# Optimization experiments

Hardware: AMD Instinct MI355X
Metric: run time of the kernel (lower is better)

## Reference

```python
import jax, jax.numpy as jnp
import numpy as np

N = 65536      # nodes
E = 262144     # edges per metapath
K = 8          # sampled edges per node
NMP = 2        # metapaths (n_mp)
DEPTH = 2      # layers
H = 4          # heads
D = 256        # prep_len / hidden (= H*PH)
PH = 64        # per-head output dim
ED = 64        # raw edge embedding dim


def setup_inputs() -> dict:
    key = jax.random.key(0)
    ks = jax.random.split(key, 16)
    s = 1.0 / np.sqrt(D)
    return {
        "feats": jax.random.normal(ks[0], (N, D), jnp.float32),
        "edge_emb": jax.random.normal(ks[1], (NMP, E, ED), jnp.float32),
        "edge_node_adj": jax.random.randint(ks[2], (NMP, E, 2), 0, N, dtype=jnp.int32),
        "node2edge_idx": jax.random.randint(ks[3], (NMP, N, K), 0, E, dtype=jnp.int32),
        "W_prep0": jax.random.normal(ks[4], (D, D), jnp.float32) * s,
        "W_prep1": jax.random.normal(ks[5], (D, D), jnp.float32) * s,
        "W_eprep": jax.random.normal(ks[6], (NMP, ED, D), jnp.float32) * (1.0 / np.sqrt(ED)),
        "a_e": jax.random.normal(ks[7], (NMP, DEPTH, H, D), jnp.float32) * s,
        "a_n": jax.random.normal(ks[8], (NMP, DEPTH, H, D), jnp.float32) * s,
        "W_e": jax.random.normal(ks[9], (NMP, DEPTH, H, D, PH), jnp.float32) * s,
        "a_s": jax.random.normal(ks[10], (NMP, DEPTH, H, D), jnp.float32) * s,
        "a_edge": jax.random.normal(ks[11], (NMP, DEPTH, H, D), jnp.float32) * s,
        "W_self": jax.random.normal(ks[12], (NMP, DEPTH, H, D, PH), jnp.float32) * s,
        "W_nb": jax.random.normal(ks[13], (NMP, DEPTH, H, D, PH), jnp.float32) * s,
    }


def _forward(feats, edge_emb, edge_node_adj, node2edge_idx,
             W_prep0, W_prep1, W_eprep, a_e, a_n, W_e, a_s, a_edge, W_self, W_nb):
    dummy = feats @ W_prep0     # prep(layer_idx=0)  [N,D]
    base = feats @ W_prep1      # prep(layer_idx=1)  [N,D]
    outputs = []
    for mp in range(NMP):
        x = base
        edges = edge_emb[mp] @ W_eprep[mp]           # [E,D]
        ena = edge_node_adj[mp]                      # [E,2]
        n2e = node2edge_idx[mp]                      # [N,K]
        skips = []
        for L in range(DEPTH):
            # --- edge aggregator: gather 2 endpoint node feats, attend, project ---
            ep = x[ena]                              # [E,2,D] gather
            s_e = jax.nn.leaky_relu(
                jnp.einsum('eqd,hd->ehq', ep, a_n[mp, L])
                + jnp.einsum('ed,hd->eh', edges, a_e[mp, L])[..., None], 0.2)  # [E,H,2]
            alp = jax.nn.softmax(s_e, axis=-1)
            agg = jnp.einsum('ehq,eqd->ehd', alp, ep)                          # [E,H,D]
            e_out = jax.nn.elu(
                jnp.einsum('ehd,hdp->ehp', edges[:, None, :] + agg, W_e[mp, L])
            ).reshape(E, H * PH)                                               # [E,D]
            # --- node aggregator: gather K sampled edge feats (OLD edges), attend ---
            xin = x if L > 0 else dummy              # layer 0 self-feature uses dummy prep
            eg = edges[n2e]                          # [N,K,D] gather
            s_n = jax.nn.leaky_relu(
                jnp.einsum('nd,hd->nh', xin, a_s[mp, L])[:, :, None]
                + jnp.einsum('nkd,hd->nhk', eg, a_edge[mp, L]), 0.2)           # [N,H,K]
            aln = jax.nn.softmax(s_n, axis=-1)
            nag = jnp.einsum('nhk,nkd->nhd', aln, eg)                          # [N,H,D]
            n_out = jax.nn.elu(
                jnp.einsum('nd,hdp->nhp', xin, W_self[mp, L])
                + jnp.einsum('nhd,hdp->nhp', nag, W_nb[mp, L])
            ).reshape(N, H * PH)                                               # [N,D]
            skips.append(n_out)
            x = n_out
            edges = e_out
        outputs.append(jnp.concatenate(skips, axis=-1))   # [N, DEPTH*D]
    return jnp.stack(outputs, axis=0)                     # [NMP, N, DEPTH*D]


def reference(feats, edge_emb, edge_node_adj, node2edge_idx,
              W_prep0, W_prep1, W_eprep, a_e, a_n, W_e, a_s, a_edge, W_self, W_nb):
    return _forward(feats, edge_emb, edge_node_adj, node2edge_idx,
                    W_prep0, W_prep1, W_eprep, a_e, a_n, W_e, a_s, a_edge, W_self, W_nb)
```

## Files before the change

kernel.cpp:

```cpp
#include <hip/hip_runtime.h>

typedef unsigned short ushort_t;
typedef unsigned int uint_t;

#define N_NODES 65536
#define N_EDGES 262144

typedef __attribute__((ext_vector_type(8))) short bf16x8;
typedef __attribute__((ext_vector_type(4))) float f32x4;

__device__ __forceinline__ ushort_t f2b(float x) {
  uint_t u = __float_as_uint(x);
  u += 0x7fffu + ((u >> 16) & 1u);
  return (ushort_t)(u >> 16);
}
__device__ __forceinline__ void dec8(uint4 v, float* f) {
  f[0] = __uint_as_float(v.x << 16); f[1] = __uint_as_float(v.x & 0xffff0000u);
  f[2] = __uint_as_float(v.y << 16); f[3] = __uint_as_float(v.y & 0xffff0000u);
  f[4] = __uint_as_float(v.z << 16); f[5] = __uint_as_float(v.z & 0xffff0000u);
  f[6] = __uint_as_float(v.w << 16); f[7] = __uint_as_float(v.w & 0xffff0000u);
}
__device__ __forceinline__ void dec4(uint2 v, float* f) {
  f[0] = __uint_as_float(v.x << 16); f[1] = __uint_as_float(v.x & 0xffff0000u);
  f[2] = __uint_as_float(v.y << 16); f[3] = __uint_as_float(v.y & 0xffff0000u);
}
__device__ __forceinline__ uint4 enc8(const float* f) {
  uint4 v;
  v.x = (uint_t)f2b(f[0]) | ((uint_t)f2b(f[1]) << 16);
  v.y = (uint_t)f2b(f[2]) | ((uint_t)f2b(f[3]) << 16);
  v.z = (uint_t)f2b(f[4]) | ((uint_t)f2b(f[5]) << 16);
  v.w = (uint_t)f2b(f[6]) | ((uint_t)f2b(f[7]) << 16);
  return v;
}
__device__ __forceinline__ uint2 enc4(const float* f) {
  uint2 v;
  v.x = (uint_t)f2b(f[0]) | ((uint_t)f2b(f[1]) << 16);
  v.y = (uint_t)f2b(f[2]) | ((uint_t)f2b(f[3]) << 16);
  return v;
}
__device__ __forceinline__ void ld8(const float* p, float* f) {
  float4 v0 = *(const float4*)p;
  float4 v1 = *(const float4*)(p + 4);
  f[0]=v0.x; f[1]=v0.y; f[2]=v0.z; f[3]=v0.w;
  f[4]=v1.x; f[5]=v1.y; f[6]=v1.z; f[7]=v1.w;
}

#define ELUF(v) ((v) > 0.f ? (v) : __expf(v) - 1.f)

__device__ __forceinline__ void async16(void* lds, const void* g) {
  __builtin_amdgcn_global_load_lds(
      (const __attribute__((address_space(1))) void*)g,
      (__attribute__((address_space(3))) void*)lds, 16, 0, 0);
}

__global__ void wt_kernel(const float* __restrict__ src, ushort_t* __restrict__ dst,
                          int K, int N) {
  long m = blockIdx.y;
  long base = m * (long)K * N;
  int tid = blockIdx.x * 256 + threadIdx.x;
  if (tid >= K * N) return;
  int k = tid % K, n = tid / K;
  dst[base + (long)n * K + k] = f2b(src[base + (long)k * N + n]);
}

__global__ __launch_bounds__(256, 2) void gemm_mfma2(
    const float* __restrict__ A, const ushort_t* __restrict__ Wt0,
    const ushort_t* __restrict__ Wt1, ushort_t* __restrict__ out0,
    ushort_t* __restrict__ out1) {
  __shared__ __align__(16) char smem[4096 + 16384 + 16384];
  ushort_t (*sA)[32]  = (ushort_t(*)[32])smem;
  ushort_t (*sB0)[32] = (ushort_t(*)[32])(smem + 4096);
  ushort_t (*sB1)[32] = (ushort_t(*)[32])(smem + 20480);
  int t = threadIdx.x, w = t >> 6, l = t & 63;
  long r0 = (long)blockIdx.x * 64;
  f32x4 zero = {0.f, 0.f, 0.f, 0.f};
  f32x4 acc0[4][4], acc1[4][4];
#pragma unroll
  for (int mt = 0; mt < 4; ++mt)
#pragma unroll
    for (int nt = 0; nt < 4; ++nt) { acc0[mt][nt] = zero; acc1[mt][nt] = zero; }

  for (int kc = 0; kc < 8; ++kc) {
    __syncthreads();
    {
      int r = t >> 2, ks8 = (t & 3) * 8;
      float f[8]; ld8(A + (r0 + r) * 256 + kc * 32 + ks8, f);
      *(uint4*)&sA[r][ks8] = enc8(f);
    }
#pragma unroll
    for (int j = 0; j < 4; ++j) {
      int u = (w * 4 + j) * 64 + l;
      int n = u >> 2, ks = u & 3;
      async16((char*)sB0 + (w * 4 + j) * 1024, Wt0 + (long)n * 256 + kc * 32 + ks * 8);
      async16((char*)sB1 + (w * 4 + j) * 1024, Wt1 + (long)n * 256 + kc * 32 + ks * 8);
    }
    __syncthreads();
    bf16x8 af[4];
#pragma unroll
    for (int mt = 0; mt < 4; ++mt)
      af[mt] = *(const bf16x8*)&sA[mt * 16 + (l & 15)][(l >> 4) * 8];
#pragma unroll
    for (int nt = 0; nt < 4; ++nt) {
      bf16x8 b0 = *(const bf16x8*)&sB0[w * 64 + nt * 16 + (l & 15)][(l >> 4) * 8];
      bf16x8 b1 = *(const bf16x8*)&sB1[w * 64 + nt * 16 + (l & 15)][(l >> 4) * 8];
#pragma unroll
      for (int mt = 0; mt < 4; ++mt) {
        acc0[mt][nt] = __builtin_amdgcn_mfma_f32_16x16x32_bf16(af[mt], b0, acc0[mt][nt], 0, 0, 0);
        acc1[mt][nt] = __builtin_amdgcn_mfma_f32_16x16x32_bf16(af[mt], b1, acc1[mt][nt], 0, 0, 0);
      }
    }
  }
#pragma unroll
  for (int mt = 0; mt < 4; ++mt)
#pragma unroll
    for (int nt = 0; nt < 4; ++nt)
#pragma unroll
      for (int i = 0; i < 4; ++i) {
        long row = r0 + mt * 16 + (l >> 4) * 4 + i;
        int col = w * 64 + nt * 16 + (l & 15);
        out0[row * 256 + col] = f2b(acc0[mt][nt][i]);
        out1[row * 256 + col] = f2b(acc1[mt][nt][i]);
      }
}

__global__ __launch_bounds__(256, 2) void gemm_eproj(
    const ushort_t* __restrict__ A, const ushort_t* __restrict__ Wt,
    const float* __restrict__ a_vec,
    ushort_t* __restrict__ outb, float* __restrict__ sco) {
  __shared__ __align__(16) char smem[4096 + 16384 + 8192];
  ushort_t (*sA)[32]   = (ushort_t(*)[32])smem;
  ushort_t (*sB)[32]   = (ushort_t(*)[32])(smem + 4096);
  ushort_t (*sAe)[256] = (ushort_t(*)[256])(smem + 20480);
  int t = threadIdx.x, w = t >> 6, l = t & 63;
  long r0 = (long)blockIdx.x * 64;

  {
    int row = t >> 4, seg = (t & 15) * 16;
    float f[16];
    if (row < 4) {
      ld8(a_vec + row * 256 + seg, f);
      ld8(a_vec + row * 256 + seg + 8, f + 8);
    } else {
#pragma unroll
      for (int i = 0; i < 16; ++i) f[i] = 0.f;
    }
    *(uint4*)&sAe[row][seg] = enc8(f);
    *(uint4*)&sAe[row][seg + 8] = enc8(f + 8);
  }

  f32x4 zero = {0.f, 0.f, 0.f, 0.f};
  f32x4 acc[4][4];
  f32x4 accs[4];
#pragma unroll
  for (int mt = 0; mt < 4; ++mt) {
    accs[mt] = zero;
#pragma unroll
    for (int nt = 0; nt < 4; ++nt) acc[mt][nt] = zero;
  }

  for (int kc = 0; kc < 8; ++kc) {
    __syncthreads();
    async16((char*)sA + w * 1024, A + (r0 + (t >> 2)) * 256 + kc * 32 + (t & 3) * 8);
#pragma unroll
    for (int j = 0; j < 4; ++j) {
      int u = (w * 4 + j) * 64 + l;
      int n = u >> 2, ks = u & 3;
      async16((char*)sB + (w * 4 + j) * 1024, Wt + (long)n * 256 + kc * 32 + ks * 8);
    }
    __syncthreads();
    bf16x8 af[4], bf[4];
#pragma unroll
    for (int mt = 0; mt < 4; ++mt)
      af[mt] = *(const bf16x8*)&sA[mt * 16 + (l & 15)][(l >> 4) * 8];
#pragma unroll
    for (int nt = 0; nt < 4; ++nt)
      bf[nt] = *(const bf16x8*)&sB[w * 64 + nt * 16 + (l & 15)][(l >> 4) * 8];
#pragma unroll
    for (int mt = 0; mt < 4; ++mt)
#pragma unroll
      for (int nt = 0; nt < 4; ++nt)
        acc[mt][nt] = __builtin_amdgcn_mfma_f32_16x16x32_bf16(af[mt], bf[nt], acc[mt][nt], 0, 0, 0);
    if (w == 0) {
      bf16x8 bs = *(const bf16x8*)&sAe[l & 15][kc * 32 + (l >> 4) * 8];
#pragma unroll
      for (int mt = 0; mt < 4; ++mt)
        accs[mt] = __builtin_amdgcn_mfma_f32_16x16x32_bf16(af[mt], bs, accs[mt], 0, 0, 0);
    }
  }
#pragma unroll
  for (int mt = 0; mt < 4; ++mt)
#pragma unroll
    for (int nt = 0; nt < 4; ++nt)
#pragma unroll
      for (int i = 0; i < 4; ++i) {
        long row = r0 + mt * 16 + (l >> 4) * 4 + i;
        int col = w * 64 + nt * 16 + (l & 15);
        outb[row * 256 + col] = f2b(acc[mt][nt][i]);
      }
  if (w == 0 && (l & 15) < 4) {
#pragma unroll
    for (int mt = 0; mt < 4; ++mt)
#pragma unroll
      for (int i = 0; i < 4; ++i) {
        long row = r0 + mt * 16 + (l >> 4) * 4 + i;
        sco[row * 4 + (l & 15)] = accs[mt][i];
      }
  }
}

__global__ __launch_bounds__(256, 2) void edge_mega(
    const float* __restrict__ eemb,
    const ushort_t* __restrict__ WtEp,
    const ushort_t* __restrict__ WtN0,
    const ushort_t* __restrict__ WtE0,
    const ushort_t* __restrict__ WtN1,
    const float* __restrict__ a_e0,
    const float* __restrict__ a_ed0,
    const float* __restrict__ a_ed1,
    const int* __restrict__ ena,
    const ushort_t* __restrict__ xprojE,
    const float* __restrict__ xan,
    ushort_t* __restrict__ eproj0, float* __restrict__ sed0,
    ushort_t* __restrict__ eprojL1, float* __restrict__ sed1) {
  __shared__ __align__(16) char smem[32768 + 16384 + 8192 + 4096 + 1024 + 2048 + 512];
  char* sEc            = smem;
  ushort_t (*sB)[32]   = (ushort_t(*)[32])(smem + 32768);
  ushort_t (*sAe)[256] = (ushort_t(*)[256])(smem + 49152);
  ushort_t (*sT)[32]   = (ushort_t(*)[32])(smem + 57344);
  float* sSea          = (float*)(smem + 61440);
  float (*sAlp)[4][2]  = (float(*)[4][2])(smem + 62464);
  int* sIdx            = (int*)(smem + 64512);
  int t = threadIdx.x, w = t >> 6, l = t & 63;
  long e0 = (long)blockIdx.x * 64;

  if (t < 128) sIdx[t] = ena[e0 * 2 + t];
  {
    int row = t >> 4, seg = (t & 15) * 16;
    float f[16];
    if (row < 8) {
      const float* src = (row < 4 ? a_e0 + row * 256 : a_ed0 + (row - 4) * 256) + seg;
      ld8(src, f); ld8(src + 8, f + 8);
    } else {
#pragma unroll
      for (int i = 0; i < 16; ++i) f[i] = 0.f;
    }
    *(uint4*)&sAe[row][seg] = enc8(f);
    *(uint4*)&sAe[row][seg + 8] = enc8(f + 8);
  }

  f32x4 zero = {0.f, 0.f, 0.f, 0.f};
  f32x4 acc[4][4];
#pragma unroll
  for (int mt = 0; mt < 4; ++mt)
#pragma unroll
    for (int nt = 0; nt < 4; ++nt) acc[mt][nt] = zero;

  for (int kc = 0; kc < 2; ++kc) {
    __syncthreads();
    {
      int r = t >> 2, ks8 = (t & 3) * 8;
      float f[8]; ld8(eemb + (e0 + r) * 64 + kc * 32 + ks8, f);
      *(uint4*)&sT[r][ks8] = enc8(f);
    }
#pragma unroll
    for (int j = 0; j < 4; ++j) {
      int u = (w * 4 + j) * 64 + l;
      int n = u >> 2, ks = u & 3;
      async16((char*)sB + (w * 4 + j) * 1024, WtEp + (long)n * 64 + kc * 32 + ks * 8);
    }
    __syncthreads();
    bf16x8 af[4], bf[4];
#pragma unroll
    for (int mt = 0; mt < 4; ++mt)
      af[mt] = *(const bf16x8*)&sT[mt * 16 + (l & 15)][(l >> 4) * 8];
#pragma unroll
    for (int nt = 0; nt < 4; ++nt)
      bf[nt] = *(const bf16x8*)&sB[w * 64 + nt * 16 + (l & 15)][(l >> 4) * 8];
#pragma unroll
    for (int mt = 0; mt < 4; ++mt)
#pragma unroll
      for (int nt = 0; nt < 4; ++nt)
        acc[mt][nt] = __builtin_amdgcn_mfma_f32_16x16x32_bf16(af[mt], bf[nt], acc[mt][nt], 0, 0, 0);
  }
#pragma unroll
  for (int mt = 0; mt < 4; ++mt)
#pragma unroll
    for (int nt = 0; nt < 4; ++nt)
#pragma unroll
      for (int i = 0; i < 4; ++i) {
        int row = mt * 16 + (l >> 4) * 4 + i;
        int col = w * 64 + nt * 16 + (l & 15);
        int cb = (col >> 3) ^ ((row & 7) << 2);
        *(ushort_t*)(sEc + row * 512 + cb * 16 + (col & 7) * 2) = f2b(acc[mt][nt][i]);
      }

  f32x4 accs[4];
#pragma unroll
  for (int mt = 0; mt < 4; ++mt) {
    accs[mt] = zero;
#pragma unroll
    for (int nt = 0; nt < 4; ++nt) acc[mt][nt] = zero;
  }
  for (int kc = 0; kc < 8; ++kc) {
    __syncthreads();
#pragma unroll
    for (int j = 0; j < 4; ++j) {
      int u = (w * 4 + j) * 64 + l;
      int n = u >> 2, ks = u & 3;
      async16((char*)sB + (w * 4 + j) * 1024, WtN0 + (long)n * 256 + kc * 32 + ks * 8);
    }
    __syncthreads();
    bf16x8 af[4], bf[4];
#pragma unroll
    for (int mt = 0; mt < 4; ++mt) {
      int row = mt * 16 + (l & 15);
      int cb = (kc * 4 + (l >> 4)) ^ ((row & 7) << 2);
      af[mt] = *(const bf16x8*)(sEc + row * 512 + cb * 16);
    }
#pragma unroll
    for (int nt = 0; nt < 4; ++nt)
      bf[nt] = *(const bf16x8*)&sB[w * 64 + nt * 16 + (l & 15)][(l >> 4) * 8];
#pragma unroll
    for (int mt = 0; mt < 4; ++mt)
#pragma unroll
      for (int nt = 0; nt < 4; ++nt)
        acc[mt][nt] = __builtin_amdgcn_mfma_f32_16x16x32_bf16(af[mt], bf[nt], acc[mt][nt], 0, 0, 0);
    if (w == 0) {
      bf16x8 bs = *(const bf16x8*)&sAe[l & 15][kc * 32 + (l >> 4) * 8];
#pragma unroll
      for (int mt = 0; mt < 4; ++mt)
        accs[mt] = __builtin_amdgcn_mfma_f32_16x16x32_bf16(af[mt], bs, accs[mt], 0, 0, 0);
    }
  }
  __syncthreads();
#pragma unroll
  for (int mt = 0; mt < 4; ++mt)
#pragma unroll
    for (int nt = 0; nt < 4; ++nt)
#pragma unroll
      for (int i = 0; i < 4; ++i) {
        long row = e0 + mt * 16 + (l >> 4) * 4 + i;
        int col = w * 64 + nt * 16 + (l & 15);
        eproj0[row * 256 + col] = f2b(acc[mt][nt][i]);
      }
  if (w == 0) {
    int c = l & 15;
#pragma unroll
    for (int mt = 0; mt < 4; ++mt)
#pragma unroll
      for (int i = 0; i < 4; ++i) {
        int row = mt * 16 + (l >> 4) * 4 + i;
        float v = accs[mt][i];
        if (c < 4) sSea[row * 4 + c] = v;
        else if (c < 8) sed0[(e0 + row) * 4 + (c - 4)] = v;
      }
  }
  {
    int row = t >> 4, seg = (t & 15) * 16;
    float f[16];
    if (row < 4) {
      ld8(a_ed1 + row * 256 + seg, f);
      ld8(a_ed1 + row * 256 + seg + 8, f + 8);
    } else {
#pragma unroll
      for (int i = 0; i < 16; ++i) f[i] = 0.f;
    }
    *(uint4*)&sAe[row][seg] = enc8(f);
    *(uint4*)&sAe[row][seg + 8] = enc8(f + 8);
  }
  __syncthreads();
  {
    int e = t >> 2, h = t & 3;
    int n0 = sIdx[2 * e], n1 = sIdx[2 * e + 1];
    float sE = sSea[e * 4 + h];
    float s0 = xan[(long)n0 * 4 + h] + sE; s0 = s0 > 0.f ? s0 : 0.2f * s0;
    float s1 = xan[(long)n1 * 4 + h] + sE; s1 = s1 > 0.f ? s1 : 0.2f * s1;
    float mx = fmaxf(s0, s1);
    float g0 = __expf(s0 - mx), g1 = __expf(s1 - mx);
    float inv = 1.f / (g0 + g1);
    sAlp[e][h][0] = g0 * inv;
    sAlp[e][h][1] = g1 * inv;
  }

#pragma unroll
  for (int mt = 0; mt < 4; ++mt)
#pragma unroll
    for (int nt = 0; nt < 4; ++nt) acc[mt][nt] = zero;
  for (int kc = 0; kc < 8; ++kc) {
    __syncthreads();
#pragma unroll
    for (int j = 0; j < 4; ++j) {
      int u = (w * 4 + j) * 64 + l;
      int n = u >> 2, ks = u & 3;
      async16((char*)sB + (w * 4 + j) * 1024, WtE0 + (long)n * 256 + kc * 32 + ks * 8);
    }
    __syncthreads();
    bf16x8 af[4], bf[4];
#pragma unroll
    for (int mt = 0; mt < 4; ++mt) {
      int row = mt * 16 + (l & 15);
      int cb = (kc * 4 + (l >> 4)) ^ ((row & 7) << 2);
      af[mt] = *(const bf16x8*)(sEc + row * 512 + cb * 16);
    }
#pragma unroll
    for (int nt = 0; nt < 4; ++nt)
      bf[nt] = *(const bf16x8*)&sB[w * 64 + nt * 16 + (l & 15)][(l >> 4) * 8];
#pragma unroll
    for (int mt = 0; mt < 4; ++mt)
#pragma unroll
      for (int nt = 0; nt < 4; ++nt)
        acc[mt][nt] = __builtin_amdgcn_mfma_f32_16x16x32_bf16(af[mt], bf[nt], acc[mt][nt], 0, 0, 0);
  }
  __syncthreads();
#pragma unroll
  for (int mt = 0; mt < 4; ++mt)
#pragma unroll
    for (int nt = 0; nt < 4; ++nt)
#pragma unroll
      for (int i = 0; i < 4; ++i) {
        int row = mt * 16 + (l >> 4) * 4 + i;
        int col = w * 64 + nt * 16 + (l & 15);
        int cb = (col >> 3) ^ ((row & 7) << 2);
        *(ushort_t*)(sEc + row * 512 + cb * 16 + (col & 7) * 2) = f2b(acc[mt][nt][i]);
      }

#pragma unroll
  for (int mt = 0; mt < 4; ++mt) {
    accs[mt] = zero;
#pragma unroll
    for (int nt = 0; nt < 4; ++nt) acc[mt][nt] = zero;
  }
  int r3 = t >> 2, cq = t & 3;
  int n0r = sIdx[2 * r3], n1r = sIdx[2 * r3 + 1];
  const ushort_t* p0 = xprojE + (long)n0r * 256 + cq * 8;
  const ushort_t* p1 = xprojE + (long)n1r * 256 + cq * 8;
  float a0h[4], a1h[4];
#pragma unroll
  for (int h = 0; h < 4; ++h) { a0h[h] = sAlp[r3][h][0]; a1h[h] = sAlp[r3][h][1]; }
  for (int kc = 0; kc < 8; ++kc) {
    __syncthreads();
#pragma unroll
    for (int j = 0; j < 4; ++j) {
      int u = (w * 4 + j) * 64 + l;
      int n = u >> 2, ks = u & 3;
      async16((char*)sB + (w * 4 + j) * 1024, WtN1 + (long)n * 256 + kc * 32 + ks * 8);
    }
    {
      int h = kc >> 1;
      int cb = (kc * 4 + cq) ^ ((r3 & 7) << 2);
      float ep[8], x0[8], x1[8], y[8];
      dec8(*(const uint4*)(sEc + r3 * 512 + cb * 16), ep);
      dec8(*(const uint4*)(p0 + kc * 32), x0);
      dec8(*(const uint4*)(p1 + kc * 32), x1);
#pragma unroll
      for (int d = 0; d < 8; ++d) {
        float v = ep[d] + a0h[h] * x0[d] + a1h[h] * x1[d];
        y[d] = ELUF(v);
      }
      *(uint4*)&sT[r3][cq * 8] = enc8(y);
    }
    __syncthreads();
    bf16x8 af[4], bf[4];
#pragma unroll
    for (int mt = 0; mt < 4; ++mt)
      af[mt] = *(const bf16x8*)&sT[mt * 16 + (l & 15)][(l >> 4) * 8];
#pragma unroll
    for (int nt = 0; nt < 4; ++nt)
      bf[nt] = *(const bf16x8*)&sB[w * 64 + nt * 16 + (l & 15)][(l >> 4) * 8];
#pragma unroll
    for (int mt = 0; mt < 4; ++mt)
#pragma unroll
      for (int nt = 0; nt < 4; ++nt)
        acc[mt][nt] = __builtin_amdgcn_mfma_f32_16x16x32_bf16(af[mt], bf[nt], acc[mt][nt], 0, 0, 0);
    if (w == 0) {
      bf16x8 bs = *(const bf16x8*)&sAe[l & 15][kc * 32 + (l >> 4) * 8];
#pragma unroll
      for (int mt = 0; mt < 4; ++mt)
        accs[mt] = __builtin_amdgcn_mfma_f32_16x16x32_bf16(af[mt], bs, accs[mt], 0, 0, 0);
    }
  }
#pragma unroll
  for (int mt = 0; mt < 4; ++mt)
#pragma unroll
    for (int nt = 0; nt < 4; ++nt)
#pragma unroll
      for (int i = 0; i < 4; ++i) {
        long row = e0 + mt * 16 + (l >> 4) * 4 + i;
        int col = w * 64 + nt * 16 + (l & 15);
        eprojL1[row * 256 + col] = f2b(acc[mt][nt][i]);
      }
  if (w == 0 && (l & 15) < 4) {
#pragma unroll
    for (int mt = 0; mt < 4; ++mt)
#pragma unroll
      for (int i = 0; i < 4; ++i) {
        long row = e0 + mt * 16 + (l >> 4) * 4 + i;
        sed1[row * 4 + (l & 15)] = accs[mt][i];
      }
  }
}

__global__ __launch_bounds__(256, 2) void node_out(
    const ushort_t* __restrict__ xb,
    const int* __restrict__ n2e,
    const ushort_t* __restrict__ eproj,
    const float* __restrict__ sed,
    const float* __restrict__ a_s,
    const ushort_t* __restrict__ WtS,
    float* __restrict__ outp,
    ushort_t* __restrict__ xout) {
  __shared__ __align__(16) char smem[33280 + 1024 + 4096 + 4096];
  ushort_t (*sX)[32]   = (ushort_t(*)[32])smem;
  ushort_t (*sBs)[32]  = (ushort_t(*)[32])(smem + 2048);
  ushort_t (*sAs)[256] = (ushort_t(*)[256])(smem + 18432);
  float* sOutF         = (float*)smem;
  int*   sIdx          = (int*)(smem + 33280);
  float* sSe           = (float*)(smem + 34304);
  float* sAln          = (float*)(smem + 38400);
  int t = threadIdx.x, w = t >> 6, l = t & 63;
  long n0 = (long)blockIdx.x * 32;

  {
    int e = n2e[n0 * 8 + t];
    sIdx[t] = e;
    *(float4*)&sSe[t * 4] = *(const float4*)(sed + (long)e * 4);
  }
  if (t < 128) {
    int row = t >> 5, dof = (t & 31) * 8;
    float f[8]; ld8(a_s + row * 256 + dof, f);
    *(uint4*)&sAs[row][dof] = enc8(f);
  }

  f32x4 zero = {0.f, 0.f, 0.f, 0.f};
  f32x4 acc[2][4];
#pragma unroll
  for (int mt = 0; mt < 2; ++mt)
#pragma unroll
    for (int nt = 0; nt < 4; ++nt) acc[mt][nt] = zero;
  float ssp = 0.f;
  int sn = t >> 3, shalf = (t & 1) * 16, sh = (t >> 1) & 3;

  for (int kc = 0; kc < 8; ++kc) {
    __syncthreads();
    if (w == 0) {
#pragma unroll
      for (int j = 0; j < 2; ++j) {
        int u = j * 64 + l;
        int r = u >> 2, ks = u & 3;
        async16((char*)sX + j * 1024, xb + (n0 + r) * 256 + kc * 32 + ks * 8);
      }
    }
#pragma unroll
    for (int j = 0; j < 4; ++j) {
      int u = (w * 4 + j) * 64 + l;
      int n = u >> 2, ks = u & 3;
      async16((char*)sBs + (w * 4 + j) * 1024, WtS + (long)n * 256 + kc * 32 + ks * 8);
    }
    __syncthreads();
    bf16x8 ax[2], bs[4];
#pragma unroll
    for (int mt = 0; mt < 2; ++mt)
      ax[mt] = *(const bf16x8*)&sX[mt * 16 + (l & 15)][(l >> 4) * 8];
#pragma unroll
    for (int nt = 0; nt < 4; ++nt)
      bs[nt] = *(const bf16x8*)&sBs[w * 64 + nt * 16 + (l & 15)][(l >> 4) * 8];
#pragma unroll
    for (int mt = 0; mt < 2; ++mt)
#pragma unroll
      for (int nt = 0; nt < 4; ++nt)
        acc[mt][nt] = __builtin_amdgcn_mfma_f32_16x16x32_bf16(ax[mt], bs[nt], acc[mt][nt], 0, 0, 0);
    {
      float xv[16], av[16];
      dec8(*(const uint4*)&sX[sn][shalf], xv);
      dec8(*(const uint4*)&sX[sn][shalf + 8], xv + 8);
      dec8(*(const uint4*)&sAs[sh][kc * 32 + shalf], av);
      dec8(*(const uint4*)&sAs[sh][kc * 32 + shalf + 8], av + 8);
#pragma unroll
      for (int d = 0; d < 16; ++d) ssp += xv[d] * av[d];
    }
  }
  __syncthreads();
#pragma unroll
  for (int mt = 0; mt < 2; ++mt)
#pragma unroll
    for (int nt = 0; nt < 4; ++nt)
#pragma unroll
      for (int i = 0; i < 4; ++i) {
        int row = mt * 16 + (l >> 4) * 4 + i;
        int col = w * 64 + nt * 16 + (l & 15);
        sOutF[row * 260 + col] = acc[mt][nt][i];
      }
  float ssv = ssp + __shfl_xor(ssp, 1, 64);
  if (!(t & 1)) {
    float sv[8], mx = -1e30f;
#pragma unroll
    for (int k = 0; k < 8; ++k) {
      float s = ssv + sSe[(sn * 8 + k) * 4 + sh];
      s = s > 0.f ? s : 0.2f * s;
      sv[k] = s; mx = fmaxf(mx, s);
    }
    float sum = 0.f;
#pragma unroll
    for (int k = 0; k < 8; ++k) { sv[k] = __expf(sv[k] - mx); sum += sv[k]; }
    float inv = 1.f / sum;
#pragma unroll
    for (int k = 0; k < 8; ++k) sAln[(sn * 4 + sh) * 8 + k] = sv[k] * inv;
  }
  __syncthreads();

  int nT = t >> 3, sT = t & 7, hh = sT >> 1, dof = sT * 32;
  float wts[8];
#pragma unroll
  for (int k = 0; k < 8; ++k) wts[k] = sAln[(nT * 4 + hh) * 8 + k];
  int eidx[8];
#pragma unroll
  for (int k = 0; k < 8; ++k) eidx[k] = sIdx[nT * 8 + k];
  float o[32];
#pragma unroll
  for (int j = 0; j < 8; ++j) {
    float4 sv = *(const float4*)&sOutF[nT * 260 + dof + j * 4];
    o[j * 4 + 0] = sv.x; o[j * 4 + 1] = sv.y; o[j * 4 + 2] = sv.z; o[j * 4 + 3] = sv.w;
  }
#pragma unroll
  for (int k = 0; k < 8; ++k) {
    const ushort_t* pr = eproj + (long)eidx[k] * 256 + dof;
    float v[32];
    dec8(*(const uint4*)(pr),      v);
    dec8(*(const uint4*)(pr + 8),  v + 8);
    dec8(*(const uint4*)(pr + 16), v + 16);
    dec8(*(const uint4*)(pr + 24), v + 24);
    float wk = wts[k];
#pragma unroll
    for (int d = 0; d < 32; ++d) o[d] += wk * v[d];
  }
  long row = n0 + nT;
  float res[32];
#pragma unroll
  for (int d = 0; d < 32; ++d) res[d] = ELUF(o[d]);
  float* po = outp + row * 512 + dof;
#pragma unroll
  for (int j = 0; j < 8; ++j) {
    float4 q;
    q.x = res[j * 4 + 0]; q.y = res[j * 4 + 1]; q.z = res[j * 4 + 2]; q.w = res[j * 4 + 3];
    *(float4*)(po + j * 4) = q;
  }
  if (xout) {
#pragma unroll
    for (int j = 0; j < 4; ++j)
      *(uint4*)(xout + row * 256 + dof + j * 8) = enc8(res + j * 8);
  }
}

extern "C" void kernel_launch(void* const* d_in, const int* in_sizes, int n_in,
                              void* d_out, int out_size, void* d_ws, size_t ws_size,
                              hipStream_t stream) {
  (void)in_sizes; (void)n_in; (void)out_size; (void)ws_size;
  const float* feats  = (const float*)d_in[0];
  const float* eemb   = (const float*)d_in[1];
  const int*   adj    = (const int*)d_in[2];
  const int*   n2e    = (const int*)d_in[3];
  const float* Wp0    = (const float*)d_in[4];
  const float* Wp1    = (const float*)d_in[5];
  const float* Wep    = (const float*)d_in[6];
  const float* a_e    = (const float*)d_in[7];
  const float* a_n    = (const float*)d_in[8];
  const float* W_e    = (const float*)d_in[9];
  const float* a_s    = (const float*)d_in[10];
  const float* a_edge = (const float*)d_in[11];
  const float* W_self = (const float*)d_in[12];
  const float* W_nb   = (const float*)d_in[13];
  float* out = (float*)d_out;

  char* w = (char*)d_ws;
  ushort_t* dummy_bf = (ushort_t*)w; w += (size_t)N_NODES * 256 * 2;
  ushort_t* base_bf  = (ushort_t*)w; w += (size_t)N_NODES * 256 * 2;
  ushort_t* eproj0   = (ushort_t*)w; w += (size_t)N_EDGES * 256 * 2;
  ushort_t* eprojL1  = (ushort_t*)w; w += (size_t)N_EDGES * 256 * 2;
  ushort_t* bufX     = (ushort_t*)w; w += (size_t)N_NODES * 256 * 2;
  float*    sed0     = (float*)w;    w += (size_t)N_EDGES * 4 * 4;
  float*    sed1     = (float*)w;    w += (size_t)N_EDGES * 4 * 4;
  float*    xan      = (float*)w;    w += (size_t)N_NODES * 4 * 4;
  ushort_t* WtP0     = (ushort_t*)w; w += 256 * 256 * 2;
  ushort_t* WtP1     = (ushort_t*)w; w += 256 * 256 * 2;
  ushort_t* WtEp     = (ushort_t*)w; w += 2 * 256 * 64 * 2;
  ushort_t* WtE      = (ushort_t*)w; w += 16 * 16384 * 2;
  ushort_t* WtS      = (ushort_t*)w; w += 16 * 16384 * 2;
  ushort_t* WtN      = (ushort_t*)w; w += 16 * 16384 * 2;

  wt_kernel<<<dim3(256, 1), 256, 0, stream>>>(Wp0, WtP0, 256, 256);
  wt_kernel<<<dim3(256, 1), 256, 0, stream>>>(Wp1, WtP1, 256, 256);
  wt_kernel<<<dim3(64, 2), 256, 0, stream>>>(Wep, WtEp, 64, 256);
  wt_kernel<<<dim3(64, 16), 256, 0, stream>>>(W_e, WtE, 256, 64);
  wt_kernel<<<dim3(64, 16), 256, 0, stream>>>(W_self, WtS, 256, 64);
  wt_kernel<<<dim3(64, 16), 256, 0, stream>>>(W_nb, WtN, 256, 64);

  gemm_mfma2<<<N_NODES / 64, 256, 0, stream>>>(feats, WtP0, WtP1, dummy_bf, base_bf);

  for (int mp = 0; mp < 2; ++mp) {
    const int* adj_mp = adj + (size_t)mp * N_EDGES * 2;
    const int* n2e_mp = n2e + (size_t)mp * N_NODES * 8;
    size_t ao0 = (size_t)(mp * 2 + 0) * 1024, ao1 = (size_t)(mp * 2 + 1) * 1024;
    size_t wo0 = (size_t)(mp * 2 + 0) * 65536, wo1 = (size_t)(mp * 2 + 1) * 65536;

    ushort_t* xprojE = bufX;
    ushort_t* xl1    = bufX;

    gemm_eproj<<<N_NODES / 64, 256, 0, stream>>>(base_bf, WtE + wo0, a_n + ao0, xprojE, xan);
    edge_mega<<<N_EDGES / 64, 256, 0, stream>>>(
        eemb + (size_t)mp * N_EDGES * 64, WtEp + (size_t)mp * 16384,
        WtN + wo0, WtE + wo0, WtN + wo1,
        a_e + ao0, a_edge + ao0, a_edge + ao1,
        adj_mp, xprojE, xan, eproj0, sed0, eprojL1, sed1);
    node_out<<<N_NODES / 32, 256, 0, stream>>>(dummy_bf, n2e_mp, eproj0, sed0,
                                               a_s + ao0, WtS + wo0,
                                               out + (size_t)mp * N_NODES * 512, xl1);
    node_out<<<N_NODES / 32, 256, 0, stream>>>(xl1, n2e_mp, eprojL1, sed1,
                                               a_s + ao1, WtS + wo1,
                                               out + (size_t)mp * N_NODES * 512 + 256,
                                               (ushort_t*)nullptr);
  }
}
```

Before: 1.442 ms.

## Fold layer-0 edge attention vectors into edge-prep weights and shrink edge_mega LDS

Precomputes W_eprep·a_e and W_eprep·a_edge in a tiny kernel, so the layer-0 edge attention scores come from the K=64 edge-prep MFMA instead of the K=256 loop. That loop only ever used L=0 attention vectors, since the mp offset is applied at launch. It also drops the index and alpha shared buffers, loads endpoint indices and xan directly into registers, reuses the sEc buffer for the ELU output, and changes the swizzle. Together these cut LDS to about 53KB so launch bounds can rise to 3 blocks per CU. The risks are extra register pressure from a second accumulator set and rounding differences, because the folded weights are stored as bf16.

```diff
diff --git a/kernel.cpp b/kernel.cpp
--- a/kernel.cpp
+++ b/kernel.cpp
@@ -19,10 +19,6 @@
   f[2] = __uint_as_float(v.y << 16); f[3] = __uint_as_float(v.y & 0xffff0000u);
   f[4] = __uint_as_float(v.z << 16); f[5] = __uint_as_float(v.z & 0xffff0000u);
   f[6] = __uint_as_float(v.w << 16); f[7] = __uint_as_float(v.w & 0xffff0000u);
-}
-__device__ __forceinline__ void dec4(uint2 v, float* f) {
-  f[0] = __uint_as_float(v.x << 16); f[1] = __uint_as_float(v.x & 0xffff0000u);
-  f[2] = __uint_as_float(v.y << 16); f[3] = __uint_as_float(v.y & 0xffff0000u);
 }
 __device__ __forceinline__ uint4 enc8(const float* f) {
   uint4 v;
@@ -30,12 +26,6 @@
   v.y = (uint_t)f2b(f[2]) | ((uint_t)f2b(f[3]) << 16);
   v.z = (uint_t)f2b(f[4]) | ((uint_t)f2b(f[5]) << 16);
   v.w = (uint_t)f2b(f[6]) | ((uint_t)f2b(f[7]) << 16);
-  return v;
-}
-__device__ __forceinline__ uint2 enc4(const float* f) {
-  uint2 v;
-  v.x = (uint_t)f2b(f[0]) | ((uint_t)f2b(f[1]) << 16);
-  v.y = (uint_t)f2b(f[2]) | ((uint_t)f2b(f[3]) << 16);
   return v;
 }
 __device__ __forceinline__ void ld8(const float* p, float* f) {
@@ -61,6 +51,24 @@
   if (tid >= K * N) return;
   int k = tid % K, n = tid / K;
   dst[base + (long)n * K + k] = f2b(src[base + (long)k * N + n]);
+}
+
+__global__ void g_kernel(const float* __restrict__ Wep, const float* __restrict__ a_e,
+                         const float* __restrict__ a_edge, ushort_t* __restrict__ gbuf) {
+  int mp = blockIdx.x;
+  int t = threadIdx.x;
+  int v = t >> 6, c = t & 63;
+  const float* vec = (v < 4 ? a_e + mp * 2048 + v * 256
+                            : a_edge + mp * 2048 + (v - 4) * 256);
+  const float* wrow = Wep + (long)mp * 64 * 256 + (long)c * 256;
+  float s = 0.f;
+#pragma unroll
+  for (int d = 0; d < 256; d += 4) {
+    float4 wv = *(const float4*)(wrow + d);
+    float4 av = *(const float4*)(vec + d);
+    s += wv.x * av.x + wv.y * av.y + wv.z * av.z + wv.w * av.w;
+  }
+  gbuf[mp * 512 + v * 64 + c] = f2b(s);
 }
 
 __global__ __launch_bounds__(256, 2) void gemm_mfma2(
@@ -208,52 +216,48 @@
   }
 }
 
-__global__ __launch_bounds__(256, 2) void edge_mega(
+__global__ __launch_bounds__(256, 3) void edge_mega(
     const float* __restrict__ eemb,
     const ushort_t* __restrict__ WtEp,
     const ushort_t* __restrict__ WtN0,
     const ushort_t* __restrict__ WtE0,
     const ushort_t* __restrict__ WtN1,
-    const float* __restrict__ a_e0,
-    const float* __restrict__ a_ed0,
+    const ushort_t* __restrict__ gbuf,
     const float* __restrict__ a_ed1,
     const int* __restrict__ ena,
     const ushort_t* __restrict__ xprojE,
     const float* __restrict__ xan,
     ushort_t* __restrict__ eproj0, float* __restrict__ sed0,
     ushort_t* __restrict__ eprojL1, float* __restrict__ sed1) {
-  __shared__ __align__(16) char smem[32768 + 16384 + 8192 + 4096 + 1024 + 2048 + 512];
+  __shared__ __align__(16) char smem[54272];
   char* sEc            = smem;
   ushort_t (*sB)[32]   = (ushort_t(*)[32])(smem + 32768);
-  ushort_t (*sAe)[256] = (ushort_t(*)[256])(smem + 49152);
-  ushort_t (*sT)[32]   = (ushort_t(*)[32])(smem + 57344);
-  float* sSea          = (float*)(smem + 61440);
-  float (*sAlp)[4][2]  = (float(*)[4][2])(smem + 62464);
-  int* sIdx            = (int*)(smem + 64512);
+  ushort_t (*sSc0)[64] = (ushort_t(*)[64])(smem + 49152);
+  ushort_t (*sT)[32]   = (ushort_t(*)[32])(smem + 50176);
+  float* sSea          = (float*)(smem + 50176);
+  ushort_t (*sEd1)[256]= (ushort_t(*)[256])(smem + 51200);
   int t = threadIdx.x, w = t >> 6, l = t & 63;
   long e0 = (long)blockIdx.x * 64;
-
-  if (t < 128) sIdx[t] = ena[e0 * 2 + t];
-  {
-    int row = t >> 4, seg = (t & 15) * 16;
-    float f[16];
-    if (row < 8) {
-      const float* src = (row < 4 ? a_e0 + row * 256 : a_ed0 + (row - 4) * 256) + seg;
-      ld8(src, f); ld8(src + 8, f + 8);
-    } else {
-#pragma unroll
-      for (int i = 0; i < 16; ++i) f[i] = 0.f;
-    }
-    *(uint4*)&sAe[row][seg] = enc8(f);
-    *(uint4*)&sAe[row][seg + 8] = enc8(f + 8);
-  }
+  bf16x8 z8 = {0, 0, 0, 0, 0, 0, 0, 0};
+
+  int r3 = t >> 2, cq = t & 3;
+  int n0r = ena[(e0 + r3) * 2 + 0];
+  int n1r = ena[(e0 + r3) * 2 + 1];
+  float4 x0s = *(const float4*)(xan + (long)n0r * 4);
+  float4 x1s = *(const float4*)(xan + (long)n1r * 4);
+
+  if (t < 64)
+    *(uint4*)&sSc0[t >> 3][(t & 7) * 8] = *(const uint4*)(gbuf + (t >> 3) * 64 + (t & 7) * 8);
 
   f32x4 zero = {0.f, 0.f, 0.f, 0.f};
   f32x4 acc[4][4];
-#pragma unroll
-  for (int mt = 0; mt < 4; ++mt)
+  f32x4 accs[4];
+#pragma unroll
+  for (int mt = 0; mt < 4; ++mt) {
+    accs[mt] = zero;
 #pragma unroll
     for (int nt = 0; nt < 4; ++nt) acc[mt][nt] = zero;
+  }
 
   for (int kc = 0; kc < 2; ++kc) {
     __syncthreads();
@@ -281,6 +285,13 @@
 #pragma unroll
       for (int nt = 0; nt < 4; ++nt)
         acc[mt][nt] = __builtin_amdgcn_mfma_f32_16x16x32_bf16(af[mt], bf[nt], acc[mt][nt], 0, 0, 0);
+    if (w == 0) {
+      bf16x8 bs = ((l & 15) < 8)
+          ? *(const bf16x8*)&sSc0[l & 15][kc * 32 + (l >> 4) * 8] : z8;
+#pragma unroll
+      for (int mt = 0; mt < 4; ++mt)
+        accs[mt] = __builtin_amdgcn_mfma_f32_16x16x32_bf16(af[mt], bs, accs[mt], 0, 0, 0);
+    }
   }
 #pragma unroll
   for (int mt = 0; mt < 4; ++mt)
@@ -290,17 +301,35 @@
       for (int i = 0; i < 4; ++i) {
         int row = mt * 16 + (l >> 4) * 4 + i;
         int col = w * 64 + nt * 16 + (l & 15);
-        int cb = (col >> 3) ^ ((row & 7) << 2);
+        int cb = (col >> 3) ^ (row & 7);
         *(ushort_t*)(sEc + row * 512 + cb * 16 + (col & 7) * 2) = f2b(acc[mt][nt][i]);
       }
-
-  f32x4 accs[4];
-#pragma unroll
-  for (int mt = 0; mt < 4; ++mt) {
-    accs[mt] = zero;
+  __syncthreads();
+
+  if (w == 0) {
+    int c = l & 15;
+    if (c < 8) {
+#pragma unroll
+      for (int mt = 0; mt < 4; ++mt)
+#pragma unroll
+        for (int i = 0; i < 4; ++i) {
+          int row = mt * 16 + (l >> 4) * 4 + i;
+          float v = accs[mt][i];
+          if (c < 4) sSea[row * 4 + c] = v;
+          else sed0[(e0 + row) * 4 + (c - 4)] = v;
+        }
+    }
+  }
+  if (t < 128) {
+    int row = t >> 5, dof = (t & 31) * 8;
+    float f[8]; ld8(a_ed1 + row * 256 + dof, f);
+    *(uint4*)&sEd1[row][dof] = enc8(f);
+  }
+
+#pragma unroll
+  for (int mt = 0; mt < 4; ++mt)
 #pragma unroll
     for (int nt = 0; nt < 4; ++nt) acc[mt][nt] = zero;
-  }
   for (int kc = 0; kc < 8; ++kc) {
     __syncthreads();
 #pragma unroll
@@ -314,7 +343,7 @@
 #pragma unroll
     for (int mt = 0; mt < 4; ++mt) {
       int row = mt * 16 + (l & 15);
-      int cb = (kc * 4 + (l >> 4)) ^ ((row & 7) << 2);
+      int cb = (kc * 4 + (l >> 4)) ^ (row & 7);
       af[mt] = *(const bf16x8*)(sEc + row * 512 + cb * 16);
     }
 #pragma unroll
@@ -325,14 +354,7 @@
 #pragma unroll
       for (int nt = 0; nt < 4; ++nt)
         acc[mt][nt] = __builtin_amdgcn_mfma_f32_16x16x32_bf16(af[mt], bf[nt], acc[mt][nt], 0, 0, 0);
-    if (w == 0) {
-      bf16x8 bs = *(const bf16x8*)&sAe[l & 15][kc * 32 + (l >> 4) * 8];
-#pragma unroll
-      for (int mt = 0; mt < 4; ++mt)
-        accs[mt] = __builtin_amdgcn_mfma_f32_16x16x32_bf16(af[mt], bs, accs[mt], 0, 0, 0);
-    }
-  }
-  __syncthreads();
+  }
 #pragma unroll
   for (int mt = 0; mt < 4; ++mt)
 #pragma unroll
@@ -343,44 +365,6 @@
         int col = w * 64 + nt * 16 + (l & 15);
         eproj0[row * 256 + col] = f2b(acc[mt][nt][i]);
       }
-  if (w == 0) {
-    int c = l & 15;
-#pragma unroll
-    for (int mt = 0; mt < 4; ++mt)
-#pragma unroll
-      for (int i = 0; i < 4; ++i) {
-        int row = mt * 16 + (l >> 4) * 4 + i;
-        float v = accs[mt][i];
-        if (c < 4) sSea[row * 4 + c] = v;
-        else if (c < 8) sed0[(e0 + row) * 4 + (c - 4)] = v;
-      }
-  }
-  {
-    int row = t >> 4, seg = (t & 15) * 16;
-    float f[16];
-    if (row < 4) {
-      ld8(a_ed1 + row * 256 + seg, f);
-      ld8(a_ed1 + row * 256 + seg + 8, f + 8);
-    } else {
-#pragma unroll
-      for (int i = 0; i < 16; ++i) f[i] = 0.f;
-    }
-    *(uint4*)&sAe[row][seg] = enc8(f);
-    *(uint4*)&sAe[row][seg + 8] = enc8(f + 8);
-  }
-  __syncthreads();
-  {
-    int e = t >> 2, h = t & 3;
-    int n0 = sIdx[2 * e], n1 = sIdx[2 * e + 1];
-    float sE = sSea[e * 4 + h];
-    float s0 = xan[(long)n0 * 4 + h] + sE; s0 = s0 > 0.f ? s0 : 0.2f * s0;
-    float s1 = xan[(long)n1 * 4 + h] + sE; s1 = s1 > 0.f ? s1 : 0.2f * s1;
-    float mx = fmaxf(s0, s1);
-    float g0 = __expf(s0 - mx), g1 = __expf(s1 - mx);
-    float inv = 1.f / (g0 + g1);
-    sAlp[e][h][0] = g0 * inv;
-    sAlp[e][h][1] = g1 * inv;
-  }
 
 #pragma unroll
   for (int mt = 0; mt < 4; ++mt)
@@ -399,7 +383,7 @@
 #pragma unroll
     for (int mt = 0; mt < 4; ++mt) {
       int row = mt * 16 + (l & 15);
-      int cb = (kc * 4 + (l >> 4)) ^ ((row & 7) << 2);
+      int cb = (kc * 4 + (l >> 4)) ^ (row & 7);
       af[mt] = *(const bf16x8*)(sEc + row * 512 + cb * 16);
     }
 #pragma unroll
@@ -420,23 +404,35 @@
       for (int i = 0; i < 4; ++i) {
         int row = mt * 16 + (l >> 4) * 4 + i;
         int col = w * 64 + nt * 16 + (l & 15);
-        int cb = (col >> 3) ^ ((row & 7) << 2);
+        int cb = (col >> 3) ^ (row & 7);
         *(ushort_t*)(sEc + row * 512 + cb * 16 + (col & 7) * 2) = f2b(acc[mt][nt][i]);
       }
 
+  float a0h[4], a1h[4];
+  {
+    float xs0[4] = {x0s.x, x0s.y, x0s.z, x0s.w};
+    float xs1[4] = {x1s.x, x1s.y, x1s.z, x1s.w};
+#pragma unroll
+    for (int h = 0; h < 4; ++h) {
+      float sE = sSea[r3 * 4 + h];
+      float s0 = xs0[h] + sE; s0 = s0 > 0.f ? s0 : 0.2f * s0;
+      float s1 = xs1[h] + sE; s1 = s1 > 0.f ? s1 : 0.2f * s1;
+      float mx = fmaxf(s0, s1);
+      float g0 = __expf(s0 - mx), g1 = __expf(s1 - mx);
+      float inv = 1.f / (g0 + g1);
+      a0h[h] = g0 * inv; a1h[h] = g1 * inv;
+    }
+  }
+
+  f32x4 accP[4][4];
 #pragma unroll
   for (int mt = 0; mt < 4; ++mt) {
     accs[mt] = zero;
 #pragma unroll
-    for (int nt = 0; nt < 4; ++nt) acc[mt][nt] = zero;
-  }
-  int r3 = t >> 2, cq = t & 3;
-  int n0r = sIdx[2 * r3], n1r = sIdx[2 * r3 + 1];
+    for (int nt = 0; nt < 4; ++nt) accP[mt][nt] = zero;
+  }
   const ushort_t* p0 = xprojE + (long)n0r * 256 + cq * 8;
   const ushort_t* p1 = xprojE + (long)n1r * 256 + cq * 8;
-  float a0h[4], a1h[4];
-#pragma unroll
-  for (int h = 0; h < 4; ++h) { a0h[h] = sAlp[r3][h][0]; a1h[h] = sAlp[r3][h][1]; }
   for (int kc = 0; kc < 8; ++kc) {
     __syncthreads();
 #pragma unroll
@@ -447,7 +443,7 @@
     }
     {
       int h = kc >> 1;
-      int cb = (kc * 4 + cq) ^ ((r3 & 7) << 2);
+      int cb = (kc * 4 + cq) ^ (r3 & 7);
       float ep[8], x0[8], x1[8], y[8];
       dec8(*(const uint4*)(sEc + r3 * 512 + cb * 16), ep);
       dec8(*(const uint4*)(p0 + kc * 32), x0);
@@ -457,13 +453,16 @@
         float v = ep[d] + a0h[h] * x0[d] + a1h[h] * x1[d];
         y[d] = ELUF(v);
       }
-      *(uint4*)&sT[r3][cq * 8] = enc8(y);
+      *(uint4*)(sEc + r3 * 512 + cb * 16) = enc8(y);
     }
     __syncthreads();
     bf16x8 af[4], bf[4];
 #pragma unroll
-    for (int mt = 0; mt < 4; ++mt)
-      af[mt] = *(const bf16x8*)&sT[mt * 16 + (l & 15)][(l >> 4) * 8];
+    for (int mt = 0; mt < 4; ++mt) {
+      int row = mt * 16 + (l & 15);
+      int cb = (kc * 4 + (l >> 4)) ^ (row & 7);
+      af[mt] = *(const bf16x8*)(sEc + row * 512 + cb * 16);
+    }
 #pragma unroll
     for (int nt = 0; nt < 4; ++nt)
       bf[nt] = *(const bf16x8*)&sB[w * 64 + nt * 16 + (l & 15)][(l >> 4) * 8];
@@ -471,9 +470,10 @@
     for (int mt = 0; mt < 4; ++mt)
 #pragma unroll
       for (int nt = 0; nt < 4; ++nt)
-        acc[mt][nt] = __builtin_amdgcn_mfma_f32_16x16x32_bf16(af[mt], bf[nt], acc[mt][nt], 0, 0, 0);
+        accP[mt][nt] = __builtin_amdgcn_mfma_f32_16x16x32_bf16(af[mt], bf[nt], accP[mt][nt], 0, 0, 0);
     if (w == 0) {
-      bf16x8 bs = *(const bf16x8*)&sAe[l & 15][kc * 32 + (l >> 4) * 8];
+      bf16x8 bs = ((l & 15) < 4)
+          ? *(const bf16x8*)&sEd1[l & 15][kc * 32 + (l >> 4) * 8] : z8;
 #pragma unroll
       for (int mt = 0; mt < 4; ++mt)
         accs[mt] = __builtin_amdgcn_mfma_f32_16x16x32_bf16(af[mt], bs, accs[mt], 0, 0, 0);
@@ -487,7 +487,7 @@
       for (int i = 0; i < 4; ++i) {
         long row = e0 + mt * 16 + (l >> 4) * 4 + i;
         int col = w * 64 + nt * 16 + (l & 15);
-        eprojL1[row * 256 + col] = f2b(acc[mt][nt][i]);
+        eprojL1[row * 256 + col] = f2b(accP[mt][nt][i]);
       }
   if (w == 0 && (l & 15) < 4) {
 #pragma unroll
@@ -680,6 +680,7 @@
   float*    sed0     = (float*)w;    w += (size_t)N_EDGES * 4 * 4;
   float*    sed1     = (float*)w;    w += (size_t)N_EDGES * 4 * 4;
   float*    xan      = (float*)w;    w += (size_t)N_NODES * 4 * 4;
+  ushort_t* gbuf     = (ushort_t*)w; w += 2 * 512 * 2;
   ushort_t* WtP0     = (ushort_t*)w; w += 256 * 256 * 2;
   ushort_t* WtP1     = (ushort_t*)w; w += 256 * 256 * 2;
   ushort_t* WtEp     = (ushort_t*)w; w += 2 * 256 * 64 * 2;
@@ -693,6 +694,7 @@
   wt_kernel<<<dim3(64, 16), 256, 0, stream>>>(W_e, WtE, 256, 64);
   wt_kernel<<<dim3(64, 16), 256, 0, stream>>>(W_self, WtS, 256, 64);
   wt_kernel<<<dim3(64, 16), 256, 0, stream>>>(W_nb, WtN, 256, 64);
+  g_kernel<<<2, 512, 0, stream>>>(Wep, a_e, a_edge, gbuf);
 
   gemm_mfma2<<<N_NODES / 64, 256, 0, stream>>>(feats, WtP0, WtP1, dummy_bf, base_bf);
 
@@ -709,7 +711,7 @@
     edge_mega<<<N_EDGES / 64, 256, 0, stream>>>(
         eemb + (size_t)mp * N_EDGES * 64, WtEp + (size_t)mp * 16384,
         WtN + wo0, WtE + wo0, WtN + wo1,
-        a_e + ao0, a_edge + ao0, a_edge + ao1,
+        gbuf + (size_t)mp * 512, a_edge + ao1,
         adj_mp, xprojE, xan, eproj0, sed0, eprojL1, sed1);
     node_out<<<N_NODES / 32, 256, 0, stream>>>(dummy_bf, n2e_mp, eproj0, sed0,
                                                a_s + ao0, WtS + wo0,
```

After: 1.900 ms. 1.32x slower.
